# Optimization experiments

Measured on AMD Instinct MI355X. Metric: run time of the kernel, lower is better.

Reference implementation:

```python
import jax, jax.numpy as jnp
import numpy as np

B, N, C = 2, 2048, 768
H = 12
D = C // H
SCALE = D ** -0.5
EPS = 1e-5
HID = 4 * C


def layer_norm(x, g, b):
    mu = jnp.mean(x, axis=-1, keepdims=True)
    var = jnp.var(x, axis=-1, keepdims=True)
    return (x - mu) * jax.lax.rsqrt(var + EPS) * g + b


def setup_inputs():
    key = jax.random.key(0)
    ks = jax.random.split(key, 12)
    s = C ** -0.5
    x = jax.random.normal(ks[0], (B, N, C), dtype=jnp.float32)
    mask = (jax.random.uniform(ks[1], (B, N, N)) < 0.1).astype(jnp.float32)
    return {
        "x": x,
        "mask": mask,
        "g1": jnp.ones((C,), jnp.float32),
        "b1": jnp.zeros((C,), jnp.float32),
        "Wq": jax.random.normal(ks[2], (C, C), jnp.float32) * s,
        "Wkv": jax.random.normal(ks[3], (2 * C, C), jnp.float32) * s,
        "Wp": jax.random.normal(ks[4], (C, C), jnp.float32) * s,
        "bp": jnp.zeros((C,), jnp.float32),
        "g2": jnp.ones((C,), jnp.float32),
        "b2": jnp.zeros((C,), jnp.float32),
        "W1": jax.random.normal(ks[5], (HID, C), jnp.float32) * s,
        "bf1": jnp.zeros((HID,), jnp.float32),
        "W2": jax.random.normal(ks[6], (C, HID), jnp.float32) * (HID ** -0.5),
        "bf2": jnpmp if False else jnp.zeros((C,), jnp.float32),
    }


def block_fwd(x, mask, g1, b1, Wq, Wkv, Wp, bp, g2, b2, W1, bf1, W2, bf2):
    # --- attention branch (pre-norm) ---
    xn = layer_norm(x, g1, b1)
    q = (xn @ Wq.T).reshape(B, N, H, D).transpose(0, 2, 1, 3)      # bhnd
    kv = (xn @ Wkv.T).reshape(B, N, 2, H, D).transpose(2, 0, 3, 1, 4)
    k, v = kv[0], kv[1]                                             # bhnd
    attn = jnp.einsum('bhnd,bhmd->bhnm', q, k) * SCALE
    attn = attn + (mask * -100000.0)[:, None]                       # additive mask
    attn = jax.nn.softmax(attn, axis=-1)
    o = jnp.einsum('bhnm,bhmd->bhnd', attn, v)
    o = o.transpose(0, 2, 1, 3).reshape(B, N, C)
    o = o @ Wp.T + bp
    x = x + o
    # --- MLP branch (pre-norm) ---
    xn2 = layer_norm(x, g2, b2)
    h = jax.nn.gelu(xn2 @ W1.T + bf1, approximate=False)
    x = x + (h @ W2.T + bf2)
    return x


def reference(x, mask, g1, b1, Wq, Wkv, Wp, bp, g2, b2, W1, bf1, W2, bf2):
    return block_fwd(x, mask, g1, b1, Wq, Wkv, Wp, bp, g2, b2, W1, bf1, W2, bf2)
```

## Files before the change

kernel.cpp:

```cpp
#include <hip/hip_runtime.h>
#include <hip/hip_bf16.h>
#include <cstdint>
#include <cstddef>

#define BB 2
#define NN 2048
#define CC 768
#define HH 12
#define DD 64
#define HID 3072
#define TT (BB*NN)

typedef __attribute__((ext_vector_type(8))) short bf16x8;
typedef __attribute__((ext_vector_type(4))) short bf16x4;
typedef __attribute__((ext_vector_type(4))) float f32x4;

__device__ __forceinline__ unsigned short f2bf(float f) {
    unsigned int u = __float_as_uint(f);
    u += 0x7fffu + ((u >> 16) & 1u);
    return (unsigned short)(u >> 16);
}
__device__ __forceinline__ float bf2f(unsigned short u) {
    return __uint_as_float(((unsigned int)u) << 16);
}
#if __has_builtin(__builtin_amdgcn_exp2f)
#define EXP2F(x) __builtin_amdgcn_exp2f(x)
#else
#define EXP2F(x) exp2f(x)
#endif

__device__ __forceinline__ void gload16(const void* g, void* l) {
    __builtin_amdgcn_global_load_lds((__attribute__((address_space(1))) unsigned int*)g,
                                     (__attribute__((address_space(3))) unsigned int*)l,
                                     16, 0, 0);
}

struct CvtArgs {
    const float* in[5];
    unsigned short* out[5];
    int n4[5];
};
typedef __attribute__((ext_vector_type(4))) float float4v;
typedef __attribute__((ext_vector_type(4))) unsigned short ushort4v;
__global__ __launch_bounds__(256) void cvt5_kernel(CvtArgs a) {
    int base = blockIdx.x * 256 + threadIdx.x;
    int stride = gridDim.x * 256;
#pragma unroll
    for (int s = 0; s < 5; ++s) {
        const float4v* ip = (const float4v*)a.in[s];
        ushort4v* op = (ushort4v*)a.out[s];
        for (int i = base; i < a.n4[s]; i += stride) {
            float4v v = ip[i];
            ushort4v o;
            o[0] = f2bf(v[0]); o[1] = f2bf(v[1]); o[2] = f2bf(v[2]); o[3] = f2bf(v[3]);
            op[i] = o;
        }
    }
}

__global__ __launch_bounds__(256) void maskbits_kernel(const float* __restrict__ mask,
                                                       unsigned short* __restrict__ mb, int n) {
    int i = blockIdx.x * 256 + threadIdx.x;
    if (i >= n) return;
    const float4v* mp = (const float4v*)(mask + (size_t)i * 16);
    unsigned int bits = 0;
#pragma unroll
    for (int q = 0; q < 4; ++q) {
        float4v v = mp[q];
#pragma unroll
        for (int j = 0; j < 4; ++j) bits |= (v[j] > 0.5f) ? (1u << (q * 4 + j)) : 0u;
    }
    mb[i] = (unsigned short)bits;
}

__global__ __launch_bounds__(256) void ln_kernel(const float* __restrict__ x,
                                                 const float* __restrict__ g,
                                                 const float* __restrict__ b,
                                                 unsigned short* __restrict__ out) {
    int t = blockIdx.x;
    int tid = threadIdx.x;
    const float* xr = x + (size_t)t * CC;
    float v0 = xr[tid], v1 = xr[tid + 256], v2 = xr[tid + 512];
    float s = v0 + v1 + v2;
    float s2 = v0 * v0 + v1 * v1 + v2 * v2;
#pragma unroll
    for (int off = 1; off < 64; off <<= 1) {
        s  += __shfl_xor(s, off);
        s2 += __shfl_xor(s2, off);
    }
    __shared__ float red[8];
    int wv = tid >> 6, lane = tid & 63;
    if (lane == 0) { red[wv] = s; red[wv + 4] = s2; }
    __syncthreads();
    s  = red[0] + red[1] + red[2] + red[3];
    s2 = red[4] + red[5] + red[6] + red[7];
    float mu   = s * (1.0f / CC);
    float var  = s2 * (1.0f / CC) - mu * mu;
    float rstd = rsqrtf(var + 1e-5f);
    unsigned short* orow = out + (size_t)t * CC;
    orow[tid]       = f2bf((v0 - mu) * rstd * g[tid]       + b[tid]);
    orow[tid + 256] = f2bf((v1 - mu) * rstd * g[tid + 256] + b[tid + 256]);
    orow[tid + 512] = f2bf((v2 - mu) * rstd * g[tid + 512] + b[tid + 512]);
}

template <int EPI, int BM>
__global__ __launch_bounds__(256) void gemm_bt(const unsigned short* __restrict__ A,
                                               const unsigned short* __restrict__ Bw,
                                               const float* __restrict__ bias,
                                               const float* __restrict__ res,
                                               void* __restrict__ out,
                                               int M, int N, int K) {
    constexpr int MI = BM / 32;
    constexpr int NCA = (BM * 4) / 256;
    __shared__ alignas(16) unsigned short As[2][BM * 32];
    __shared__ alignas(16) unsigned short Bs[2][128 * 32];
    int tid = threadIdx.x;
    int lane = tid & 63, wv = tid >> 6;
    int l16 = lane & 15, lg = lane >> 4;
    int bm = blockIdx.x, bn = blockIdx.y;
    int wm = (wv & 1) * (BM / 2), wn = (wv >> 1) * 64;

    const unsigned short* Ab = A + (size_t)bm * BM * K;
    const unsigned short* Bb = Bw + (size_t)bn * 128 * K;

    const unsigned short* aSrc[NCA]; int aDst[NCA];
#pragma unroll
    for (int i = 0; i < NCA; ++i) {
        int c = tid + i * 256;
        int row = c >> 2, p = c & 3;
        int lc = p ^ ((row >> 1) & 3);
        aSrc[i] = Ab + (size_t)row * K + lc * 8;
        aDst[i] = c * 8;
    }
    const unsigned short* bSrc[2]; int bDst[2];
#pragma unroll
    for (int i = 0; i < 2; ++i) {
        int c = tid + i * 256;
        int row = c >> 2, p = c & 3;
        int lc = p ^ ((row >> 1) & 3);
        bSrc[i] = Bb + (size_t)row * K + lc * 8;
        bDst[i] = c * 8;
    }
    int aoff = (wm + l16) * 32 + ((lg ^ (((wm + l16) >> 1) & 3)) * 8);
    int boff = (wn + l16) * 32 + ((lg ^ (((wn + l16) >> 1) & 3)) * 8);

    f32x4 acc[MI][4];
#pragma unroll
    for (int i = 0; i < MI; ++i)
#pragma unroll
        for (int j = 0; j < 4; ++j) acc[i][j] = f32x4{0.f, 0.f, 0.f, 0.f};

    auto STAGE = [&](int s, int k0) {
#pragma unroll
        for (int i = 0; i < NCA; ++i) gload16(aSrc[i] + k0, &As[s][aDst[i]]);
#pragma unroll
        for (int i = 0; i < 2; ++i)   gload16(bSrc[i] + k0, &Bs[s][bDst[i]]);
    };

    STAGE(0, 0);
    __syncthreads();
    int nt = K / 32;
    for (int t = 0; t < nt; ++t) {
        int cur = t & 1;
        if (t + 1 < nt) STAGE(cur ^ 1, (t + 1) * 32);
        bf16x8 af[MI], bfr[4];
#pragma unroll
        for (int mi = 0; mi < MI; ++mi) af[mi]  = *(const bf16x8*)&As[cur][aoff + mi * 512];
#pragma unroll
        for (int ni = 0; ni < 4; ++ni)  bfr[ni] = *(const bf16x8*)&Bs[cur][boff + ni * 512];
#pragma unroll
        for (int mi = 0; mi < MI; ++mi)
#pragma unroll
            for (int ni = 0; ni < 4; ++ni)
                acc[mi][ni] = __builtin_amdgcn_mfma_f32_16x16x32_bf16(af[mi], bfr[ni], acc[mi][ni], 0, 0, 0);
        __syncthreads();
    }

#pragma unroll
    for (int ni = 0; ni < 4; ++ni) {
        int col = bn * 128 + wn + ni * 16 + l16;
        float bv = (EPI == 0) ? 0.f : bias[col];
#pragma unroll
        for (int mi = 0; mi < MI; ++mi) {
#pragma unroll
            for (int r = 0; r < 4; ++r) {
                int row = bm * BM + wm + mi * 16 + lg * 4 + r;
                float v = acc[mi][ni][r];
                size_t idx = (size_t)row * N + col;
                if (EPI == 0) {
                    ((unsigned short*)out)[idx] = f2bf(v);
                } else if (EPI == 1) {
                    ((float*)out)[idx] = v + bv + res[idx];
                } else if (EPI == 2) {
                    v += bv;
                    v = 0.5f * v * (1.0f + erff(v * 0.70710678118f));
                    ((unsigned short*)out)[idx] = f2bf(v);
                } else {
                    ((float*)out)[idx] = v + bv + res[idx];
                }
            }
        }
    }
}

#define KVB 64
#define ANT (NN/KVB)
#define VP 68
__global__ __launch_bounds__(512) void attn_kernel(const unsigned short* __restrict__ qkv,
                                                   const unsigned short* __restrict__ maskb,
                                                   unsigned short* __restrict__ o) {
    __shared__ alignas(16) unsigned short Ks[2][64 * 64];
    __shared__ alignas(16) unsigned short Vt[2][64 * VP];
    int tid = threadIdx.x;
    int lane = tid & 63, wv = tid >> 6;
    int l16 = lane & 15, lg = lane >> 4;
    int qb = blockIdx.x;
    int bh = blockIdx.y;
    int b = bh / HH, h = bh % HH;
    int qrow = qb * 128 + wv * 16 + l16;

    const unsigned short* qp = qkv + ((size_t)(b * NN + qrow)) * 2304 + h * DD;
    bf16x8 q0r = *(const bf16x8*)(qp + 8 * lg);
    bf16x8 q1r = *(const bf16x8*)(qp + 32 + 8 * lg);
    const float QSC = 0.125f * 1.4426950408889634f;
    bf16x8 q0, q1;
#pragma unroll
    for (int j = 0; j < 8; ++j) {
        q0[j] = (short)f2bf(bf2f((unsigned short)q0r[j]) * QSC);
        q1[j] = (short)f2bf(bf2f((unsigned short)q1r[j]) * QSC);
    }

    const unsigned short* mrow  = maskb + ((size_t)(b * NN + qrow)) * 128;
    const unsigned short* kbase = qkv + (size_t)b * NN * 2304 + 768 + h * DD;
    const unsigned short* vbase = qkv + (size_t)b * NN * 2304 + 1536 + h * DD;

    int k_row = tid >> 3, k_p = tid & 7;
    int k_lc = k_p ^ (k_row & 7);
    const unsigned short* kSrc = kbase + (size_t)k_row * 2304 + k_lc * 8;
    int kp = tid & 31, dg = tid >> 5;
    const unsigned short* vSrc = vbase + (size_t)(2 * kp) * 2304 + dg * 4;

    int sw = l16 & 7;
    int kb0 = l16 * 64 + ((lg ^ sw) * 8);
    int kb1 = l16 * 64 + (((lg + 4) ^ sw) * 8);
    int vbo = l16 * VP + lg * 4;

    bf16x4 va, vb;
    unsigned long long mb_cur, mb_nxt;

    f32x4 oa[4];
#pragma unroll
    for (int i = 0; i < 4; ++i) oa[i] = f32x4{0.f, 0.f, 0.f, 0.f};
    float mrun = -INFINITY, lrun = 0.f;

    auto LOAD = [&](int t, int s) {
        gload16(kSrc + (size_t)t * KVB * 2304, &Ks[s][tid * 8]);
        const unsigned short* vp = vSrc + (size_t)t * KVB * 2304;
        va = *(const bf16x4*)(vp);
        vb = *(const bf16x4*)(vp + 2304);
        mb_nxt = *(const unsigned long long*)(mrow + t * 4);
    };
    auto WRITEV = [&](int s) {
        unsigned int* VtU = (unsigned int*)Vt[s];
#pragma unroll
        for (int j = 0; j < 4; ++j)
            VtU[(dg * 4 + j) * (VP / 2) + kp] =
                (unsigned int)(unsigned short)va[j] | ((unsigned int)(unsigned short)vb[j] << 16);
    };

    LOAD(0, 0);
    WRITEV(0);
    mb_cur = mb_nxt;
    __syncthreads();
    int cur = 0;

    for (int kt = 0; kt < ANT; ++kt) {
        bool pre = (kt + 1 < ANT);
        if (pre) LOAD(kt + 1, cur ^ 1);
        const unsigned short* Ksc = Ks[cur];
        const unsigned short* Vtc = Vt[cur];

        float sv[16];
#pragma unroll
        for (int ks = 0; ks < 4; ++ks) {
            bf16x8 k0 = *(const bf16x8*)&Ksc[kb0 + ks * 1024];
            bf16x8 k1 = *(const bf16x8*)&Ksc[kb1 + ks * 1024];
            f32x4 sa = f32x4{0.f, 0.f, 0.f, 0.f};
            sa = __builtin_amdgcn_mfma_f32_16x16x32_bf16(k0, q0, sa, 0, 0, 0);
            sa = __builtin_amdgcn_mfma_f32_16x16x32_bf16(k1, q1, sa, 0, 0, 0);
            unsigned int m16 = (unsigned int)(mb_cur >> (ks * 16 + lg * 4));
#pragma unroll
            for (int r = 0; r < 4; ++r) {
                float mbit = (float)((m16 >> r) & 1u);
                sv[ks * 4 + r] = fmaf(mbit, -144269.5f, sa[r]);
            }
        }
        float tmax = sv[0];
#pragma unroll
        for (int i = 1; i < 16; ++i) tmax = fmaxf(tmax, sv[i]);
        tmax = fmaxf(tmax, __shfl_xor(tmax, 16));
        tmax = fmaxf(tmax, __shfl_xor(tmax, 32));

        if (__any(tmax > mrun + 11.5f)) {
            float mnew = fmaxf(mrun, tmax);
            float sc = EXP2F(mrun - mnew);
            lrun *= sc;
#pragma unroll
            for (int db = 0; db < 4; ++db) {
                oa[db][0] *= sc; oa[db][1] *= sc; oa[db][2] *= sc; oa[db][3] *= sc;
            }
            mrun = mnew;
        }

        float ps = 0.f;
        bf16x4 pf[4];
#pragma unroll
        for (int ks = 0; ks < 4; ++ks)
#pragma unroll
            for (int r = 0; r < 4; ++r) {
                float p = EXP2F(sv[ks * 4 + r] - mrun);
                ps += p;
                pf[ks][r] = (short)f2bf(p);
            }
        lrun += ps;

#pragma unroll
        for (int ks = 0; ks < 4; ++ks)
#pragma unroll
            for (int db = 0; db < 4; ++db) {
                bf16x4 vf = *(const bf16x4*)&Vtc[vbo + db * 16 * VP + ks * 16];
                oa[db] = __builtin_amdgcn_mfma_f32_16x16x16bf16_1k(vf, pf[ks], oa[db], 0, 0, 0);
            }

        if (pre) WRITEV(cur ^ 1);
        __syncthreads();
        if (pre) { cur ^= 1; mb_cur = mb_nxt; }
    }

    float lt = lrun;
    lt += __shfl_xor(lt, 16);
    lt += __shfl_xor(lt, 32);
    float inv = 1.0f / lt;
    unsigned short* op = o + ((size_t)(b * NN + qrow)) * CC + h * DD;
#pragma unroll
    for (int db = 0; db < 4; ++db) {
        bf16x4 ov;
#pragma unroll
        for (int r = 0; r < 4; ++r) ov[r] = (short)f2bf(oa[db][r] * inv);
        *(bf16x4*)&op[db * 16 + lg * 4] = ov;
    }
}

extern "C" void kernel_launch(void* const* d_in, const int* in_sizes, int n_in,
                              void* d_out, int out_size, void* d_ws, size_t ws_size,
                              hipStream_t stream) {
    const float* x    = (const float*)d_in[0];
    const float* mask = (const float*)d_in[1];
    const float* g1   = (const float*)d_in[2];
    const float* b1   = (const float*)d_in[3];
    const float* Wq   = (const float*)d_in[4];
    const float* Wkv  = (const float*)d_in[5];
    const float* Wp   = (const float*)d_in[6];
    const float* bp   = (const float*)d_in[7];
    const float* g2   = (const float*)d_in[8];
    const float* b2   = (const float*)d_in[9];
    const float* W1   = (const float*)d_in[10];
    const float* bf1  = (const float*)d_in[11];
    const float* W2   = (const float*)d_in[12];
    const float* bf2  = (const float*)d_in[13];
    float* out = (float*)d_out;

    char* w = (char*)d_ws;
    unsigned short* wqkv = (unsigned short*)w;      w += (size_t)2304 * 768 * 2;
    unsigned short* wp   = (unsigned short*)w;      w += (size_t)768 * 768 * 2;
    unsigned short* w1   = (unsigned short*)w;      w += (size_t)3072 * 768 * 2;
    unsigned short* w2   = (unsigned short*)w;      w += (size_t)768 * 3072 * 2;
    unsigned short* xn   = (unsigned short*)w;      w += (size_t)TT * CC * 2;
    unsigned short* qkv  = (unsigned short*)w;      w += (size_t)TT * 2304 * 2;
    unsigned short* mb   = (unsigned short*)w;      w += (size_t)BB * NN * 128 * 2;
    unsigned short* obuf = (unsigned short*)w;      w += (size_t)TT * CC * 2;
    float*          x1   = (float*)w;               w += (size_t)TT * CC * 4;
    unsigned short* xn2  = (unsigned short*)w;      w += (size_t)TT * CC * 2;
    unsigned short* hbuf = (unsigned short*)w;      w += (size_t)TT * HID * 2;

    CvtArgs ca;
    ca.in[0] = Wq;  ca.out[0] = wqkv;             ca.n4[0] = 768 * 768 / 4;
    ca.in[1] = Wkv; ca.out[1] = wqkv + 768 * 768; ca.n4[1] = 1536 * 768 / 4;
    ca.in[2] = Wp;  ca.out[2] = wp;               ca.n4[2] = 768 * 768 / 4;
    ca.in[3] = W1;  ca.out[3] = w1;               ca.n4[3] = 3072 * 768 / 4;
    ca.in[4] = W2;  ca.out[4] = w2;               ca.n4[4] = 768 * 3072 / 4;
    cvt5_kernel<<<1024, 256, 0, stream>>>(ca);

    {
        int n = BB * NN * (NN / 16);
        maskbits_kernel<<<(n + 255) / 256, 256, 0, stream>>>(mask, mb, n);
    }

    ln_kernel<<<TT, 256, 0, stream>>>(x, g1, b1, xn);

    gemm_bt<0, 128><<<dim3(TT / 128, 2304 / 128), 256, 0, stream>>>(xn, wqkv, nullptr, nullptr, qkv, TT, 2304, 768);

    attn_kernel<<<dim3(NN / 128, BB * HH), 512, 0, stream>>>(qkv, mb, obuf);

    gemm_bt<1, 64><<<dim3(TT / 64, 768 / 128), 256, 0, stream>>>(obuf, wp, bp, x, x1, TT, 768, 768);

    ln_kernel<<<TT, 256, 0, stream>>>(x1, g2, b2, xn2);

    gemm_bt<2, 128><<<dim3(TT / 128, HID / 128), 256, 0, stream>>>(xn2, w1, bf1, nullptr, hbuf, TT, HID, 768);

    gemm_bt<3, 64><<<dim3(TT / 64, 768 / 128), 256, 0, stream>>>(hbuf, w2, bf2, x1, out, TT, 768, HID);
}
```

Baseline: 228.1 us.

## Use finer vmcnt waits in GEMM, vectorize epilogue, shrink attention blocks

The GEMM main loop swaps __syncthreads for explicit vmcnt/lgkmcnt waits plus s_barrier. This lets the next stage's async LDS loads stay in flight while the current tile is consumed. MFMA operands are swapped so each lane holds four consecutive columns, which allows vectorized bf16x4/f32x4 epilogue stores, bias loads and residual loads. The attention kernel drops to 256 threads and 64 query rows per block, with each thread loading twice as much K/V, to give more blocks and higher occupancy at the cost of more K/V reloads across blocks.

```diff
diff --git a/kernel.cpp b/kernel.cpp
--- a/kernel.cpp
+++ b/kernel.cpp
@@ -34,6 +34,9 @@
                                      (__attribute__((address_space(3))) unsigned int*)l,
                                      16, 0, 0);
 }
+
+#define WAITV(N) asm volatile("s_waitcnt vmcnt(" #N ")" ::: "memory")
+#define WAITLGKM asm volatile("s_waitcnt lgkmcnt(0)" ::: "memory")
 
 struct CvtArgs {
     const float* in[5];
@@ -158,11 +161,16 @@
     };
 
     STAGE(0, 0);
-    __syncthreads();
     int nt = K / 32;
     for (int t = 0; t < nt; ++t) {
         int cur = t & 1;
-        if (t + 1 < nt) STAGE(cur ^ 1, (t + 1) * 32);
+        if (t + 1 < nt) {
+            STAGE(cur ^ 1, (t + 1) * 32);
+            if constexpr (NCA + 2 == 4) { WAITV(4); } else { WAITV(3); }
+        } else {
+            WAITV(0);
+        }
+        __builtin_amdgcn_s_barrier();
         bf16x8 af[MI], bfr[4];
 #pragma unroll
         for (int mi = 0; mi < MI; ++mi) af[mi]  = *(const bf16x8*)&As[cur][aoff + mi * 512];
@@ -172,32 +180,41 @@
         for (int mi = 0; mi < MI; ++mi)
 #pragma unroll
             for (int ni = 0; ni < 4; ++ni)
-                acc[mi][ni] = __builtin_amdgcn_mfma_f32_16x16x32_bf16(af[mi], bfr[ni], acc[mi][ni], 0, 0, 0);
-        __syncthreads();
-    }
-
-#pragma unroll
-    for (int ni = 0; ni < 4; ++ni) {
-        int col = bn * 128 + wn + ni * 16 + l16;
-        float bv = (EPI == 0) ? 0.f : bias[col];
-#pragma unroll
-        for (int mi = 0; mi < MI; ++mi) {
-#pragma unroll
-            for (int r = 0; r < 4; ++r) {
-                int row = bm * BM + wm + mi * 16 + lg * 4 + r;
-                float v = acc[mi][ni][r];
-                size_t idx = (size_t)row * N + col;
-                if (EPI == 0) {
-                    ((unsigned short*)out)[idx] = f2bf(v);
-                } else if (EPI == 1) {
-                    ((float*)out)[idx] = v + bv + res[idx];
-                } else if (EPI == 2) {
-                    v += bv;
-                    v = 0.5f * v * (1.0f + erff(v * 0.70710678118f));
-                    ((unsigned short*)out)[idx] = f2bf(v);
-                } else {
-                    ((float*)out)[idx] = v + bv + res[idx];
+                acc[mi][ni] = __builtin_amdgcn_mfma_f32_16x16x32_bf16(bfr[ni], af[mi], acc[mi][ni], 0, 0, 0);
+        WAITLGKM;
+        __builtin_amdgcn_s_barrier();
+    }
+
+#pragma unroll
+    for (int mi = 0; mi < MI; ++mi) {
+        int row = bm * BM + wm + mi * 16 + l16;
+#pragma unroll
+        for (int ni = 0; ni < 4; ++ni) {
+            int col = bn * 128 + wn + ni * 16 + lg * 4;
+            size_t idx = (size_t)row * N + col;
+            f32x4 v = acc[mi][ni];
+            if (EPI == 0) {
+                bf16x4 ov;
+#pragma unroll
+                for (int r = 0; r < 4; ++r) ov[r] = (short)f2bf(v[r]);
+                *(bf16x4*)((unsigned short*)out + idx) = ov;
+            } else if (EPI == 1 || EPI == 3) {
+                f32x4 bv = *(const f32x4*)&bias[col];
+                f32x4 rv = *(const f32x4*)&res[idx];
+                f32x4 ov;
+#pragma unroll
+                for (int r = 0; r < 4; ++r) ov[r] = v[r] + bv[r] + rv[r];
+                *(f32x4*)((float*)out + idx) = ov;
+            } else {
+                f32x4 bv = *(const f32x4*)&bias[col];
+                bf16x4 ov;
+#pragma unroll
+                for (int r = 0; r < 4; ++r) {
+                    float t2 = v[r] + bv[r];
+                    t2 = 0.5f * t2 * (1.0f + erff(t2 * 0.70710678118f));
+                    ov[r] = (short)f2bf(t2);
                 }
+                *(bf16x4*)((unsigned short*)out + idx) = ov;
             }
         }
     }
@@ -206,9 +223,9 @@
 #define KVB 64
 #define ANT (NN/KVB)
 #define VP 68
-__global__ __launch_bounds__(512) void attn_kernel(const unsigned short* __restrict__ qkv,
-                                                   const unsigned short* __restrict__ maskb,
-                                                   unsigned short* __restrict__ o) {
+__global__ __launch_bounds__(256, 4) void attn_kernel(const unsigned short* __restrict__ qkv,
+                                                      const unsigned short* __restrict__ maskb,
+                                                      unsigned short* __restrict__ o) {
     __shared__ alignas(16) unsigned short Ks[2][64 * 64];
     __shared__ alignas(16) unsigned short Vt[2][64 * VP];
     int tid = threadIdx.x;
@@ -217,7 +234,7 @@
     int qb = blockIdx.x;
     int bh = blockIdx.y;
     int b = bh / HH, h = bh % HH;
-    int qrow = qb * 128 + wv * 16 + l16;
+    int qrow = qb * 64 + wv * 16 + l16;
 
     const unsigned short* qp = qkv + ((size_t)(b * NN + qrow)) * 2304 + h * DD;
     bf16x8 q0r = *(const bf16x8*)(qp + 8 * lg);
@@ -234,18 +251,24 @@
     const unsigned short* kbase = qkv + (size_t)b * NN * 2304 + 768 + h * DD;
     const unsigned short* vbase = qkv + (size_t)b * NN * 2304 + 1536 + h * DD;
 
-    int k_row = tid >> 3, k_p = tid & 7;
-    int k_lc = k_p ^ (k_row & 7);
-    const unsigned short* kSrc = kbase + (size_t)k_row * 2304 + k_lc * 8;
+    const unsigned short* kSrc[2]; int kDst[2];
+#pragma unroll
+    for (int i = 0; i < 2; ++i) {
+        int c = tid + i * 256;
+        int row = c >> 3, p = c & 7;
+        int lc = p ^ (row & 7);
+        kSrc[i] = kbase + (size_t)row * 2304 + lc * 8;
+        kDst[i] = c * 8;
+    }
     int kp = tid & 31, dg = tid >> 5;
-    const unsigned short* vSrc = vbase + (size_t)(2 * kp) * 2304 + dg * 4;
+    const unsigned short* vSrc = vbase + (size_t)(2 * kp) * 2304 + dg * 8;
 
     int sw = l16 & 7;
     int kb0 = l16 * 64 + ((lg ^ sw) * 8);
     int kb1 = l16 * 64 + (((lg + 4) ^ sw) * 8);
     int vbo = l16 * VP + lg * 4;
 
-    bf16x4 va, vb;
+    bf16x8 va, vb;
     unsigned long long mb_cur, mb_nxt;
 
     f32x4 oa[4];
@@ -254,17 +277,18 @@
     float mrun = -INFINITY, lrun = 0.f;
 
     auto LOAD = [&](int t, int s) {
-        gload16(kSrc + (size_t)t * KVB * 2304, &Ks[s][tid * 8]);
+#pragma unroll
+        for (int i = 0; i < 2; ++i) gload16(kSrc[i] + (size_t)t * KVB * 2304, &Ks[s][kDst[i]]);
         const unsigned short* vp = vSrc + (size_t)t * KVB * 2304;
-        va = *(const bf16x4*)(vp);
-        vb = *(const bf16x4*)(vp + 2304);
+        va = *(const bf16x8*)(vp);
+        vb = *(const bf16x8*)(vp + 2304);
         mb_nxt = *(const unsigned long long*)(mrow + t * 4);
     };
     auto WRITEV = [&](int s) {
         unsigned int* VtU = (unsigned int*)Vt[s];
 #pragma unroll
-        for (int j = 0; j < 4; ++j)
-            VtU[(dg * 4 + j) * (VP / 2) + kp] =
+        for (int j = 0; j < 8; ++j)
+            VtU[(dg * 8 + j) * (VP / 2) + kp] =
                 (unsigned int)(unsigned short)va[j] | ((unsigned int)(unsigned short)vb[j] << 16);
     };
 
@@ -400,7 +424,7 @@
 
     gemm_bt<0, 128><<<dim3(TT / 128, 2304 / 128), 256, 0, stream>>>(xn, wqkv, nullptr, nullptr, qkv, TT, 2304, 768);
 
-    attn_kernel<<<dim3(NN / 128, BB * HH), 512, 0, stream>>>(qkv, mb, obuf);
+    attn_kernel<<<dim3(NN / 64, BB * HH), 256, 0, stream>>>(qkv, mb, obuf);
 
     gemm_bt<1, 64><<<dim3(TT / 64, 768 / 128), 256, 0, stream>>>(obuf, wp, bp, x, x1, TT, 768, 768);
 
```

Result: faster. 219.9 us (-3.6%).
